# Optimization experiments

Measured on AMD Instinct MI355X. Metric: run time of the kernel, lower is better.

Reference implementation:

```python
import jax, jax.numpy as jnp
import numpy as np

NUM_HEADS = 8
NUM_GROUPS = 32
EPS = 1e-5


def group_norm(x, gamma, beta):
    b, c, h, w = x.shape
    xg = x.reshape(b, NUM_GROUPS, c // NUM_GROUPS, h, w)
    mean = jnp.mean(xg, axis=(2, 3, 4), keepdims=True)
    var = jnp.var(xg, axis=(2, 3, 4), keepdims=True)
    xn = ((xg - mean) * jax.lax.rsqrt(var + EPS)).reshape(b, c, h, w)
    return xn * gamma[None, :, None, None] + beta[None, :, None, None]


def setup_inputs() -> dict:
    key = jax.random.key(0)
    ks = jax.random.split(key, 4)
    b, c, h, w = 16, 512, 32, 32
    x = jax.random.normal(ks[0], (b, c, h, w), dtype=jnp.float32)
    gn_gamma = jnp.ones((c,), dtype=jnp.float32)
    gn_beta = jnp.zeros((c,), dtype=jnp.float32)
    qkv_w = jax.random.normal(ks[1], (3 * c, c), dtype=jnp.float32) * (1.0 / np.sqrt(c))
    qkv_b = jnp.zeros((3 * c,), dtype=jnp.float32)
    proj_w = jax.random.normal(ks[2], (c, c), dtype=jnp.float32) * (1.0 / np.sqrt(c))
    proj_b = jnp.zeros((c,), dtype=jnp.float32)
    return {"x": x, "gn_gamma": gn_gamma, "gn_beta": gn_beta,
            "qkv_w": qkv_w, "qkv_b": qkv_b, "proj_w": proj_w, "proj_b": proj_b}


def reference(x, gn_gamma, gn_beta, qkv_w, qkv_b, proj_w, proj_b):
    b, c, h, w = x.shape
    hd = c // NUM_HEADS
    hw = h * w

    xn = group_norm(x, gn_gamma, gn_beta)
    # 1x1 conv == channel matmul
    qkv = jnp.einsum('oc,bchw->bohw', qkv_w, xn) + qkv_b[None, :, None, None]
    q, k, v = jnp.split(qkv, 3, axis=1)
    q = q.reshape(b, NUM_HEADS, hd, hw)
    k = k.reshape(b, NUM_HEADS, hd, hw)
    v = v.reshape(b, NUM_HEADS, hd, hw)

    scale = 1.0 / np.sqrt(hd)
    attn = jnp.einsum('bhdt,bhds->bhts', q, k) * scale  # [b,H,hw,hw]
    attn = jax.nn.softmax(attn, axis=-1)
    h_attn = jnp.einsum('bhts,bhds->bhdt', attn, v).reshape(b, c, h, w)

    h_attn = jnp.einsum('oc,bchw->bohw', proj_w, h_attn) + proj_b[None, :, None, None]
    return x + h_attn
```

## Files before the change

kernel.cpp:

```cpp
#include <hip/hip_runtime.h>
#include <math.h>

#define NUM_HEADS 8
#define NUM_GROUPS 32
#define EPS 1e-5f

constexpr int B  = 16;
constexpr int C  = 512;
constexpr int HW = 1024;
constexpr int HD = 64;

typedef short bf16x8 __attribute__((ext_vector_type(8)));
typedef float f32x4  __attribute__((ext_vector_type(4)));

#define QSCALE 0.1803368801111f

__device__ inline unsigned short f2bf(float f) {
    union { float f; unsigned int u; } v; v.f = f;
    unsigned int r = (v.u + 0x7FFFu + ((v.u >> 16) & 1u)) >> 16;
    return (unsigned short)r;
}

__device__ __forceinline__ unsigned int pack_trunc(float lo, float hi) {
    return __builtin_amdgcn_perm(__float_as_uint(hi), __float_as_uint(lo), 0x07060302u);
}

__device__ __forceinline__ float exp2_raw(float x) {
#if __has_builtin(__builtin_amdgcn_exp2f)
    return __builtin_amdgcn_exp2f(x);
#else
    float r; asm("v_exp_f32 %0, %1" : "=v"(r) : "v"(x)); return r;
#endif
}

__device__ __forceinline__ void gld_lds16(void* lds, const void* g) {
    __builtin_amdgcn_global_load_lds(
        (const __attribute__((address_space(1))) void*)g,
        (__attribute__((address_space(3))) void*)lds, 16, 0, 0);
}

__device__ __forceinline__ void pl32_swap(unsigned int& a, unsigned int& b) {
#if __has_builtin(__builtin_amdgcn_permlane32_swap)
    auto r = __builtin_amdgcn_permlane32_swap(a, b, false, false);
    a = r[0]; b = r[1];
#else
    asm volatile("v_permlane32_swap_b32 %0, %1" : "+v"(a), "+v"(b));
#endif
}
__device__ __forceinline__ void pl16_swap(unsigned int& a, unsigned int& b) {
#if __has_builtin(__builtin_amdgcn_permlane16_swap)
    auto r = __builtin_amdgcn_permlane16_swap(a, b, false, false);
    a = r[0]; b = r[1];
#else
    asm volatile("v_permlane16_swap_b32 %0, %1" : "+v"(a), "+v"(b));
#endif
}

#define ABAR(VM) do {                                                   \
    asm volatile("s_waitcnt vmcnt(" VM ")\n\ts_barrier" ::: "memory");  \
    __builtin_amdgcn_sched_barrier(0);                                  \
} while (0)

__global__ __launch_bounds__(256)
void groupnorm_t_kernel(const float* __restrict__ x,
                        const float* __restrict__ gamma,
                        const float* __restrict__ beta,
                        unsigned short* __restrict__ xnT) {
    const int bg = blockIdx.x;
    const int b = bg >> 5, g = bg & 31;
    const size_t base = ((size_t)b * C + (size_t)g * 16) * HW;

    float v[4][16];
    float sum = 0.f, sumsq = 0.f;
    #pragma unroll
    for (int p = 0; p < 4; ++p) {
        const int t = threadIdx.x + p * 256;
        #pragma unroll
        for (int cl = 0; cl < 16; ++cl) {
            const float f = x[base + (size_t)cl * HW + t];
            v[p][cl] = f;
            sum += f;
            sumsq += f * f;
        }
    }
    #pragma unroll
    for (int off = 32; off > 0; off >>= 1) {
        sum   += __shfl_down(sum, off, 64);
        sumsq += __shfl_down(sumsq, off, 64);
    }
    __shared__ float s_sum[4], s_sq[4];
    const int wid = threadIdx.x >> 6, lane = threadIdx.x & 63;
    if (lane == 0) { s_sum[wid] = sum; s_sq[wid] = sumsq; }
    __syncthreads();
    const float tsum = s_sum[0] + s_sum[1] + s_sum[2] + s_sum[3];
    const float tsq  = s_sq[0] + s_sq[1] + s_sq[2] + s_sq[3];
    const float mean = tsum * (1.0f / 16384.f);
    const float var  = tsq * (1.0f / 16384.f) - mean * mean;
    const float rstd = rsqrtf(var + EPS);

    float ga[16], be[16];
    #pragma unroll
    for (int cl = 0; cl < 16; ++cl) {
        ga[cl] = gamma[g * 16 + cl] * rstd;
        be[cl] = beta[g * 16 + cl] - mean * ga[cl];
    }

    #pragma unroll
    for (int p = 0; p < 4; ++p) {
        const int t = threadIdx.x + p * 256;
        unsigned short pk[16];
        #pragma unroll
        for (int cl = 0; cl < 16; ++cl)
            pk[cl] = f2bf(v[p][cl] * ga[cl] + be[cl]);
        unsigned short* dst = xnT + ((size_t)(b * 1024 + t)) * 512 + g * 16;
        *(uint4*)dst = *(const uint4*)pk;
        *(uint4*)(dst + 8) = *(const uint4*)(pk + 8);
    }
}

__global__ __launch_bounds__(256)
void wconv_kernel(const float* __restrict__ qkv_w,
                  const float* __restrict__ proj_w,
                  unsigned short* __restrict__ wqb) {
    const int i = blockIdx.x * 256 + threadIdx.x;
    const int n1 = 786432 / 4;
    const int nt = 1048576 / 4;
    if (i >= nt) return;
    const float4 v = (i < n1) ? ((const float4*)qkv_w)[i]
                              : ((const float4*)proj_w)[i - n1];
    ushort4 r;
    r.x = f2bf(v.x); r.y = f2bf(v.y); r.z = f2bf(v.z); r.w = f2bf(v.w);
    ((ushort4*)wqb)[i] = r;
}

__device__ __forceinline__ void gemm_stage(const char* __restrict__ Ab,
                                           const char* __restrict__ Bb,
                                           int step, unsigned short* As,
                                           unsigned short* Bs,
                                           int w, int lrow, int lkc) {
    #pragma unroll
    for (int i = 0; i < 2; ++i) {
        const int row = w * 32 + i * 16 + lrow;
        const int kc = lkc ^ ((row >> 1) & 3);
        const size_t goff = (size_t)row * 1024 + (size_t)step * 64 + kc * 16;
        gld_lds16((char*)As + w * 2048 + i * 1024, Ab + goff);
        gld_lds16((char*)Bs + w * 2048 + i * 1024, Bb + goff);
    }
}

__device__ __forceinline__ void gemm_step(const unsigned short* __restrict__ As,
                                          const unsigned short* __restrict__ Bs,
                                          f32x4 acc[4][4],
                                          int lo, int q4, int wm, int wn) {
    bf16x8 af[4], bfr[4];
    #pragma unroll
    for (int i = 0; i < 4; ++i) {
        const int ra = wm * 64 + i * 16 + lo;
        af[i]  = *(const bf16x8*)(As + ra * 32 + (q4 ^ ((ra >> 1) & 3)) * 8);
        const int rb = wn * 64 + i * 16 + lo;
        bfr[i] = *(const bf16x8*)(Bs + rb * 32 + (q4 ^ ((rb >> 1) & 3)) * 8);
    }
    __builtin_amdgcn_s_setprio(1);
    #pragma unroll
    for (int mi = 0; mi < 4; ++mi)
        #pragma unroll
        for (int ni = 0; ni < 4; ++ni)
            acc[mi][ni] = __builtin_amdgcn_mfma_f32_16x16x32_bf16(
                af[mi], bfr[ni], acc[mi][ni], 0, 0, 0);
    __builtin_amdgcn_s_setprio(0);
}

__device__ __forceinline__ void mfma_gemm_pipe(const char* __restrict__ Ab,
                                               const char* __restrict__ Bb,
                                               unsigned short* S,
                                               f32x4 acc[4][4]) {
    const int tid = threadIdx.x;
    const int w = tid >> 6, lane = tid & 63;
    const int lo = lane & 15, q4 = lane >> 4;
    const int wm = w >> 1, wn = w & 1;
    const int lrow = lane >> 2, lkc = lane & 3;

    unsigned short* A0 = S;             unsigned short* B0 = S + 4096;
    unsigned short* A1 = S + 8192;      unsigned short* B1 = S + 12288;
    unsigned short* A2 = S + 16384;     unsigned short* B2 = S + 20480;

    gemm_stage(Ab, Bb, 0, A0, B0, w, lrow, lkc);
    gemm_stage(Ab, Bb, 1, A1, B1, w, lrow, lkc);
    ABAR("4");
    gemm_stage(Ab, Bb, 2, A2, B2, w, lrow, lkc);
    gemm_step(A0, B0, acc, lo, q4, wm, wn);

    #pragma unroll 1
    for (int ii = 0; ii < 4; ++ii) {
        const int i = 3 * ii + 1;
        ABAR("4");
        gemm_stage(Ab, Bb, i + 2, A0, B0, w, lrow, lkc);
        gemm_step(A1, B1, acc, lo, q4, wm, wn);
        ABAR("4");
        gemm_stage(Ab, Bb, i + 3, A1, B1, w, lrow, lkc);
        gemm_step(A2, B2, acc, lo, q4, wm, wn);
        ABAR("4");
        gemm_stage(Ab, Bb, i + 4, A2, B2, w, lrow, lkc);
        gemm_step(A0, B0, acc, lo, q4, wm, wn);
    }

    ABAR("4");
    gemm_stage(Ab, Bb, 15, A0, B0, w, lrow, lkc);
    gemm_step(A1, B1, acc, lo, q4, wm, wn);
    ABAR("4");
    gemm_step(A2, B2, acc, lo, q4, wm, wn);
    ABAR("0");
    gemm_step(A0, B0, acc, lo, q4, wm, wn);
}

__global__ __launch_bounds__(256)
void qkv_mfma_kernel(const unsigned short* __restrict__ wqb,
                     const unsigned short* __restrict__ xnT,
                     const float* __restrict__ qkv_b,
                     unsigned short* __restrict__ Qt,
                     unsigned short* __restrict__ Kt,
                     unsigned short* __restrict__ Vb) {
    __shared__ __align__(16) unsigned short SMEM[3 * 8192];
    const int batch = blockIdx.z;
    const int mBase = blockIdx.y * 128, nBase = blockIdx.x * 128;

    f32x4 acc[4][4] = {};
    mfma_gemm_pipe((const char*)(wqb + (size_t)mBase * 512),
                   (const char*)(xnT + ((size_t)batch * 1024 + nBase) * 512),
                   SMEM, acc);

    const int tid = threadIdx.x;
    const int w = tid >> 6, lane = tid & 63;
    const int lo = lane & 15, q4 = lane >> 4;
    const int wm = w >> 1, wn = w & 1;
    const int mw = mBase + wm * 64;
    const int tb = nBase + wn * 64;

    __syncthreads();

    if (mw < 1024) {
        const bool isQ = mw < 512;
        const int head = (mw >> 6) & 7;
        unsigned short* dst = (isQ ? Qt : Kt) + (((size_t)batch * 8 + head) << 16);
        const float sc = isQ ? QSCALE : 1.0f;
        #pragma unroll
        for (int mi = 0; mi < 4; ++mi) {
            const float4 bq = *(const float4*)(qkv_b + mw + mi * 16 + q4 * 4);
            #pragma unroll
            for (int ni = 0; ni < 4; ++ni) {
                const int t = tb + ni * 16 + lo;
                ushort4 pk;
                pk.x = f2bf((acc[mi][ni][0] + bq.x) * sc);
                pk.y = f2bf((acc[mi][ni][1] + bq.y) * sc);
                pk.z = f2bf((acc[mi][ni][2] + bq.z) * sc);
                pk.w = f2bf((acc[mi][ni][3] + bq.w) * sc);
                *(ushort4*)(dst + (size_t)t * 64 + mi * 16 + q4 * 4) = pk;
            }
        }
    } else {
        unsigned short* T = SMEM + w * 2048;
        unsigned short* Vrow = Vb + (size_t)batch * 524288 + (size_t)(mw - 1024) * 1024 + tb;
        const int rl8 = lane >> 3, c8 = lane & 7;
        #pragma unroll
        for (int p = 0; p < 2; ++p) {
            #pragma unroll
            for (int mi2 = 0; mi2 < 2; ++mi2) {
                const int mi = 2 * p + mi2;
                const float4 bq = *(const float4*)(qkv_b + mw + mi * 16 + q4 * 4);
                const int dl = mi2 * 16 + q4 * 4;
                #pragma unroll
                for (int ni = 0; ni < 4; ++ni) {
                    const int tl = ni * 16 + lo;
                    T[(dl + 0) * 64 + tl] = f2bf(acc[mi][ni][0] + bq.x);
                    T[(dl + 1) * 64 + tl] = f2bf(acc[mi][ni][1] + bq.y);
                    T[(dl + 2) * 64 + tl] = f2bf(acc[mi][ni][2] + bq.z);
                    T[(dl + 3) * 64 + tl] = f2bf(acc[mi][ni][3] + bq.w);
                }
            }
            #pragma unroll
            for (int i = 0; i < 4; ++i) {
                const int dl = i * 8 + rl8;
                const uint4 val = *(const uint4*)&T[dl * 64 + c8 * 8];
                *(uint4*)(Vrow + (size_t)(p * 32 + dl) * 1024 + c8 * 8) = val;
            }
        }
    }
}

__device__ __forceinline__ void attn_stage(const unsigned short* __restrict__ Kp,
                                           const unsigned short* __restrict__ Vp,
                                           int s0, unsigned short* Kd,
                                           unsigned short* Vd,
                                           int w, int rl, int p8) {
    #pragma unroll
    for (int cc = 0; cc < 2; ++cc) {
        const int r = 16 * w + 8 * cc + rl;
        const int jj = p8 ^ (r & 7);
        gld_lds16(Kd + (16 * w + 8 * cc) * 64, Kp + (size_t)(s0 + r) * 64 + jj * 8);
        gld_lds16(Vd + (16 * w + 8 * cc) * 64, Vp + (size_t)r * 1024 + s0 + jj * 8);
    }
}

__device__ __forceinline__ void attn_chunk(const unsigned short* __restrict__ Kc,
                                           const unsigned short* __restrict__ Vc,
                                           const bf16x8 (&qf)[2][2],
                                           f32x4 (&oacc)[4][2], float (&lrun)[2],
                                           int lo, int q4, int xr) {
    f32x4 sacc[4][2] = {};
    __builtin_amdgcn_s_setprio(1);
    #pragma unroll
    for (int mt = 0; mt < 4; ++mt) {
        const unsigned short* kr = Kc + (16 * mt + lo) * 64;
        const bf16x8 a0 = *(const bf16x8*)(kr + ((q4    ) ^ xr) * 8);
        const bf16x8 a1 = *(const bf16x8*)(kr + ((q4 + 4) ^ xr) * 8);
        #pragma unroll
        for (int nt = 0; nt < 2; ++nt) {
            sacc[mt][nt] = __builtin_amdgcn_mfma_f32_16x16x32_bf16(a0, qf[nt][0], sacc[mt][nt], 0, 0, 0);
            sacc[mt][nt] = __builtin_amdgcn_mfma_f32_16x16x32_bf16(a1, qf[nt][1], sacc[mt][nt], 0, 0, 0);
        }
    }
    __builtin_amdgcn_s_setprio(0);

    bf16x8 bp[2][2];
    #pragma unroll
    for (int nt = 0; nt < 2; ++nt) {
        unsigned int X[4][2];
        float ps = 0.f;
        #pragma unroll
        for (int mt = 0; mt < 4; ++mt) {
            const f32x4 s = sacc[mt][nt];
            const float p0 = exp2_raw(s[0]);
            const float p1 = exp2_raw(s[1]);
            const float p2 = exp2_raw(s[2]);
            const float p3 = exp2_raw(s[3]);
            ps += (p0 + p1) + (p2 + p3);
            X[mt][0] = pack_trunc(p0, p1);
            X[mt][1] = pack_trunc(p2, p3);
        }
        lrun[nt] += ps;
        #pragma unroll
        for (int h2 = 0; h2 < 2; ++h2) {
            unsigned int Y0, Y1, Y2, Y3;
            {
                unsigned int a = X[2 * h2][0], bb = X[2 * h2 + 1][0];
                pl32_swap(a, bb);
                pl16_swap(a, bb);
                Y0 = a; Y2 = bb;
            }
            {
                unsigned int a = X[2 * h2][1], bb = X[2 * h2 + 1][1];
                pl32_swap(a, bb);
                pl16_swap(a, bb);
                Y1 = a; Y3 = bb;
            }
            union { unsigned int u[4]; bf16x8 v; } cv;
            cv.u[0] = Y0; cv.u[1] = Y1; cv.u[2] = Y2; cv.u[3] = Y3;
            bp[nt][h2] = cv.v;
        }
    }

    __builtin_amdgcn_s_setprio(1);
    #pragma unroll
    for (int md = 0; md < 4; ++md) {
        const unsigned short* vr = Vc + (16 * md + lo) * 64;
        const bf16x8 v0 = *(const bf16x8*)(vr + ((q4    ) ^ xr) * 8);
        const bf16x8 v1 = *(const bf16x8*)(vr + ((q4 + 4) ^ xr) * 8);
        #pragma unroll
        for (int nt = 0; nt < 2; ++nt) {
            oacc[md][nt] = __builtin_amdgcn_mfma_f32_16x16x32_bf16(v0, bp[nt][0], oacc[md][nt], 0, 0, 0);
            oacc[md][nt] = __builtin_amdgcn_mfma_f32_16x16x32_bf16(v1, bp[nt][1], oacc[md][nt], 0, 0, 0);
        }
    }
    __builtin_amdgcn_s_setprio(0);
}

__global__ __launch_bounds__(256, 3)
void attn_mfma_kernel(const unsigned short* __restrict__ Qt,
                      const unsigned short* __restrict__ Kt,
                      const unsigned short* __restrict__ Vb,
                      unsigned short* __restrict__ attnT) {
    const int bh = blockIdx.x;
    const int b = bh >> 3, h = bh & 7;
    const int tBase = blockIdx.y * 128;
    const int tid = threadIdx.x;
    const int w = tid >> 6, lane = tid & 63;
    const int lo = lane & 15, q4 = lane >> 4;
    const int xr = lo & 7;

    __shared__ __align__(16) unsigned short Ks[3][64 * 64];
    __shared__ __align__(16) unsigned short Vs[3][64 * 64];

    const unsigned short* Kp = Kt + ((size_t)bh << 16);
    const unsigned short* Vp = Vb + ((size_t)b * 512 + h * 64) * 1024;

    bf16x8 qf[2][2];
    {
        const unsigned short* Qp = Qt + ((size_t)bh * 1024 + tBase + 32 * w) * 64;
        #pragma unroll
        for (int nt = 0; nt < 2; ++nt) {
            qf[nt][0] = *(const bf16x8*)(Qp + (size_t)(16 * nt + lo) * 64 + 8 * q4);
            qf[nt][1] = *(const bf16x8*)(Qp + (size_t)(16 * nt + lo) * 64 + 32 + 8 * q4);
        }
    }

    const int rl = lane >> 3, p8 = lane & 7;

    f32x4 oacc[4][2] = {};
    float lrun[2] = {0.f, 0.f};

    attn_stage(Kp, Vp, 0 * 64, Ks[0], Vs[0], w, rl, p8);
    attn_stage(Kp, Vp, 1 * 64, Ks[1], Vs[1], w, rl, p8);

    ABAR("4");
    attn_stage(Kp, Vp, 2 * 64, Ks[2], Vs[2], w, rl, p8);
    attn_chunk(Ks[0], Vs[0], qf, oacc, lrun, lo, q4, xr);

    #pragma unroll 1
    for (int ii = 0; ii < 4; ++ii) {
        const int i = 3 * ii + 1;
        ABAR("4");
        attn_stage(Kp, Vp, (i + 2) * 64, Ks[0], Vs[0], w, rl, p8);
        attn_chunk(Ks[1], Vs[1], qf, oacc, lrun, lo, q4, xr);
        ABAR("4");
        attn_stage(Kp, Vp, (i + 3) * 64, Ks[1], Vs[1], w, rl, p8);
        attn_chunk(Ks[2], Vs[2], qf, oacc, lrun, lo, q4, xr);
        ABAR("4");
        attn_stage(Kp, Vp, (i + 4) * 64, Ks[2], Vs[2], w, rl, p8);
        attn_chunk(Ks[0], Vs[0], qf, oacc, lrun, lo, q4, xr);
    }

    ABAR("4");
    attn_stage(Kp, Vp, 15 * 64, Ks[0], Vs[0], w, rl, p8);
    attn_chunk(Ks[1], Vs[1], qf, oacc, lrun, lo, q4, xr);
    ABAR("4");
    attn_chunk(Ks[2], Vs[2], qf, oacc, lrun, lo, q4, xr);
    ABAR("0");
    attn_chunk(Ks[0], Vs[0], qf, oacc, lrun, lo, q4, xr);

    #pragma unroll
    for (int nt = 0; nt < 2; ++nt) {
        float lt = lrun[nt];
        lt += __shfl_xor(lt, 16, 64);
        lt += __shfl_xor(lt, 32, 64);
        const float inv = 1.0f / lt;
        const int t = tBase + 32 * w + 16 * nt + lo;
        unsigned short* op = attnT + ((size_t)(b * 1024 + t)) * 512 + h * 64;
        #pragma unroll
        for (int md = 0; md < 4; ++md) {
            uint2 pk;
            pk.x = pack_trunc(oacc[md][nt][0] * inv, oacc[md][nt][1] * inv);
            pk.y = pack_trunc(oacc[md][nt][2] * inv, oacc[md][nt][3] * inv);
            *(uint2*)(op + 16 * md + 4 * q4) = pk;
        }
    }
}

__global__ __launch_bounds__(256)
void proj_mfma_kernel(const unsigned short* __restrict__ wpb,
                      const unsigned short* __restrict__ attnT,
                      const float* __restrict__ proj_b,
                      const float* __restrict__ x,
                      float* __restrict__ out) {
    __shared__ __align__(16) unsigned short SMEM[3 * 8192];
    const int batch = blockIdx.z;
    const int mBase = blockIdx.y * 128, nBase = blockIdx.x * 128;

    f32x4 acc[4][4] = {};
    mfma_gemm_pipe((const char*)(wpb + (size_t)mBase * 512),
                   (const char*)(attnT + ((size_t)batch * 1024 + nBase) * 512),
                   SMEM, acc);

    const int tid = threadIdx.x;
    const int w = tid >> 6, lane = tid & 63;
    const int lo = lane & 15, q4 = lane >> 4;
    const int wm = w >> 1, wn = w & 1;
    const float* xb = x + (size_t)batch * 524288;
    float* ob = out + (size_t)batch * 524288;

    #pragma unroll
    for (int mi = 0; mi < 4; ++mi) {
        const int m0 = mBase + wm * 64 + mi * 16 + q4 * 4;
        const float4 bq = *(const float4*)(proj_b + m0);
        #pragma unroll
        for (int ni = 0; ni < 4; ++ni) {
            const int t = nBase + wn * 64 + ni * 16 + lo;
            const size_t o0 = (size_t)m0 * 1024 + t;
            ob[o0]          = acc[mi][ni][0] + bq.x + xb[o0];
            ob[o0 + 1024]   = acc[mi][ni][1] + bq.y + xb[o0 + 1024];
            ob[o0 + 2048]   = acc[mi][ni][2] + bq.z + xb[o0 + 2048];
            ob[o0 + 3072]   = acc[mi][ni][3] + bq.w + xb[o0 + 3072];
        }
    }
}

extern "C" void kernel_launch(void* const* d_in, const int* in_sizes, int n_in,
                              void* d_out, int out_size, void* d_ws, size_t ws_size,
                              hipStream_t stream) {
    const float* x        = (const float*)d_in[0];
    const float* gn_gamma = (const float*)d_in[1];
    const float* gn_beta  = (const float*)d_in[2];
    const float* qkv_w    = (const float*)d_in[3];
    const float* qkv_b    = (const float*)d_in[4];
    const float* proj_w   = (const float*)d_in[5];
    const float* proj_b   = (const float*)d_in[6];
    float* out = (float*)d_out;

    char* wsc = (char*)d_ws;
    unsigned short* xnT   = (unsigned short*)(wsc);
    unsigned short* Qt    = (unsigned short*)(wsc + 16777216);
    unsigned short* Kt    = (unsigned short*)(wsc + 33554432);
    unsigned short* Vb    = (unsigned short*)(wsc + 50331648);
    unsigned short* attnT = (unsigned short*)(wsc + 67108864);
    unsigned short* wqb   = (unsigned short*)(wsc + 83886080);
    unsigned short* wpb   = wqb + 786432;

    groupnorm_t_kernel<<<B * NUM_GROUPS, 256, 0, stream>>>(x, gn_gamma, gn_beta, xnT);

    wconv_kernel<<<1024, 256, 0, stream>>>(qkv_w, proj_w, wqb);

    {
        dim3 grid(HW / 128, (3 * C) / 128, B);
        qkv_mfma_kernel<<<grid, 256, 0, stream>>>(wqb, xnT, qkv_b, Qt, Kt, Vb);
    }

    {
        dim3 grid(B * NUM_HEADS, HW / 128);
        attn_mfma_kernel<<<grid, 256, 0, stream>>>(Qt, Kt, Vb, attnT);
    }

    {
        dim3 grid(HW / 128, C / 128, B);
        proj_mfma_kernel<<<grid, 256, 0, stream>>>(wpb, attnT, proj_b, x, out);
    }
}
```

Before: 206.1 us.

## Fuse groupnorm with weight conversion and shrink attention V staging buffers

The groupnorm and weight bf16-conversion kernels are merged into one launch, with extra blocks doing the weight conversion, to save a launch and let the two run concurrently. The attention kernel now stages K two chunks ahead but V only one chunk ahead, using a 3-deep K ring and a 2-deep V ring. This cuts LDS use so launch bounds can rise from 3 to 4 blocks per CU, trading a shallower V prefetch and a more intricate buffer rotation for higher occupancy.

```diff
diff --git a/kernel.cpp b/kernel.cpp
--- a/kernel.cpp
+++ b/kernel.cpp
@@ -62,10 +62,25 @@
 } while (0)
 
 __global__ __launch_bounds__(256)
-void groupnorm_t_kernel(const float* __restrict__ x,
-                        const float* __restrict__ gamma,
-                        const float* __restrict__ beta,
-                        unsigned short* __restrict__ xnT) {
+void fused_pre_kernel(const float* __restrict__ x,
+                      const float* __restrict__ gamma,
+                      const float* __restrict__ beta,
+                      unsigned short* __restrict__ xnT,
+                      const float* __restrict__ qkv_w,
+                      const float* __restrict__ proj_w,
+                      unsigned short* __restrict__ wqb) {
+    if (blockIdx.x >= 512) {
+        const int i = (blockIdx.x - 512) * 256 + threadIdx.x;
+        const int n1 = 786432 / 4;
+        const int nt = 1048576 / 4;
+        if (i >= nt) return;
+        const float4 v = (i < n1) ? ((const float4*)qkv_w)[i]
+                                  : ((const float4*)proj_w)[i - n1];
+        ushort4 r;
+        r.x = f2bf(v.x); r.y = f2bf(v.y); r.z = f2bf(v.z); r.w = f2bf(v.w);
+        ((ushort4*)wqb)[i] = r;
+        return;
+    }
     const int bg = blockIdx.x;
     const int b = bg >> 5, g = bg & 31;
     const size_t base = ((size_t)b * C + (size_t)g * 16) * HW;
@@ -116,21 +131,6 @@
         *(uint4*)dst = *(const uint4*)pk;
         *(uint4*)(dst + 8) = *(const uint4*)(pk + 8);
     }
-}
-
-__global__ __launch_bounds__(256)
-void wconv_kernel(const float* __restrict__ qkv_w,
-                  const float* __restrict__ proj_w,
-                  unsigned short* __restrict__ wqb) {
-    const int i = blockIdx.x * 256 + threadIdx.x;
-    const int n1 = 786432 / 4;
-    const int nt = 1048576 / 4;
-    if (i >= nt) return;
-    const float4 v = (i < n1) ? ((const float4*)qkv_w)[i]
-                              : ((const float4*)proj_w)[i - n1];
-    ushort4 r;
-    r.x = f2bf(v.x); r.y = f2bf(v.y); r.z = f2bf(v.z); r.w = f2bf(v.w);
-    ((ushort4*)wqb)[i] = r;
 }
 
 __device__ __forceinline__ void gemm_stage(const char* __restrict__ Ab,
@@ -287,16 +287,23 @@
     }
 }
 
-__device__ __forceinline__ void attn_stage(const unsigned short* __restrict__ Kp,
-                                           const unsigned short* __restrict__ Vp,
-                                           int s0, unsigned short* Kd,
-                                           unsigned short* Vd,
-                                           int w, int rl, int p8) {
+__device__ __forceinline__ void stage_K(const unsigned short* __restrict__ Kp,
+                                        int s0, unsigned short* Kd,
+                                        int w, int rl, int p8) {
     #pragma unroll
     for (int cc = 0; cc < 2; ++cc) {
         const int r = 16 * w + 8 * cc + rl;
         const int jj = p8 ^ (r & 7);
         gld_lds16(Kd + (16 * w + 8 * cc) * 64, Kp + (size_t)(s0 + r) * 64 + jj * 8);
+    }
+}
+__device__ __forceinline__ void stage_V(const unsigned short* __restrict__ Vp,
+                                        int s0, unsigned short* Vd,
+                                        int w, int rl, int p8) {
+    #pragma unroll
+    for (int cc = 0; cc < 2; ++cc) {
+        const int r = 16 * w + 8 * cc + rl;
+        const int jj = p8 ^ (r & 7);
         gld_lds16(Vd + (16 * w + 8 * cc) * 64, Vp + (size_t)r * 1024 + s0 + jj * 8);
     }
 }
@@ -374,7 +381,7 @@
     __builtin_amdgcn_s_setprio(0);
 }
 
-__global__ __launch_bounds__(256, 3)
+__global__ __launch_bounds__(256, 4)
 void attn_mfma_kernel(const unsigned short* __restrict__ Qt,
                       const unsigned short* __restrict__ Kt,
                       const unsigned short* __restrict__ Vb,
@@ -388,7 +395,7 @@
     const int xr = lo & 7;
 
     __shared__ __align__(16) unsigned short Ks[3][64 * 64];
-    __shared__ __align__(16) unsigned short Vs[3][64 * 64];
+    __shared__ __align__(16) unsigned short Vs[2][64 * 64];
 
     const unsigned short* Kp = Kt + ((size_t)bh << 16);
     const unsigned short* Vp = Vb + ((size_t)b * 512 + h * 64) * 1024;
@@ -408,34 +415,53 @@
     f32x4 oacc[4][2] = {};
     float lrun[2] = {0.f, 0.f};
 
-    attn_stage(Kp, Vp, 0 * 64, Ks[0], Vs[0], w, rl, p8);
-    attn_stage(Kp, Vp, 1 * 64, Ks[1], Vs[1], w, rl, p8);
-
-    ABAR("4");
-    attn_stage(Kp, Vp, 2 * 64, Ks[2], Vs[2], w, rl, p8);
+    stage_V(Vp, 0 * 64, Vs[0], w, rl, p8);
+    stage_K(Kp, 0 * 64, Ks[0], w, rl, p8);
+    stage_K(Kp, 1 * 64, Ks[1], w, rl, p8);
+
+    ABAR("2");
+    stage_V(Vp, 1 * 64, Vs[1], w, rl, p8);
+    stage_K(Kp, 2 * 64, Ks[2], w, rl, p8);
     attn_chunk(Ks[0], Vs[0], qf, oacc, lrun, lo, q4, xr);
 
     #pragma unroll 1
-    for (int ii = 0; ii < 4; ++ii) {
-        const int i = 3 * ii + 1;
-        ABAR("4");
-        attn_stage(Kp, Vp, (i + 2) * 64, Ks[0], Vs[0], w, rl, p8);
+    for (int ii = 0; ii < 2; ++ii) {
+        const int i = 6 * ii + 1;
+        ABAR("2");
+        stage_V(Vp, (i + 1) * 64, Vs[0], w, rl, p8);
+        stage_K(Kp, (i + 2) * 64, Ks[0], w, rl, p8);
         attn_chunk(Ks[1], Vs[1], qf, oacc, lrun, lo, q4, xr);
-        ABAR("4");
-        attn_stage(Kp, Vp, (i + 3) * 64, Ks[1], Vs[1], w, rl, p8);
-        attn_chunk(Ks[2], Vs[2], qf, oacc, lrun, lo, q4, xr);
-        ABAR("4");
-        attn_stage(Kp, Vp, (i + 4) * 64, Ks[2], Vs[2], w, rl, p8);
+        ABAR("2");
+        stage_V(Vp, (i + 2) * 64, Vs[1], w, rl, p8);
+        stage_K(Kp, (i + 3) * 64, Ks[1], w, rl, p8);
+        attn_chunk(Ks[2], Vs[0], qf, oacc, lrun, lo, q4, xr);
+        ABAR("2");
+        stage_V(Vp, (i + 3) * 64, Vs[0], w, rl, p8);
+        stage_K(Kp, (i + 4) * 64, Ks[2], w, rl, p8);
+        attn_chunk(Ks[0], Vs[1], qf, oacc, lrun, lo, q4, xr);
+        ABAR("2");
+        stage_V(Vp, (i + 4) * 64, Vs[1], w, rl, p8);
+        stage_K(Kp, (i + 5) * 64, Ks[0], w, rl, p8);
+        attn_chunk(Ks[1], Vs[0], qf, oacc, lrun, lo, q4, xr);
+        ABAR("2");
+        stage_V(Vp, (i + 5) * 64, Vs[0], w, rl, p8);
+        stage_K(Kp, (i + 6) * 64, Ks[1], w, rl, p8);
+        attn_chunk(Ks[2], Vs[1], qf, oacc, lrun, lo, q4, xr);
+        ABAR("2");
+        stage_V(Vp, (i + 6) * 64, Vs[1], w, rl, p8);
+        stage_K(Kp, (i + 7) * 64, Ks[2], w, rl, p8);
         attn_chunk(Ks[0], Vs[0], qf, oacc, lrun, lo, q4, xr);
     }
 
-    ABAR("4");
-    attn_stage(Kp, Vp, 15 * 64, Ks[0], Vs[0], w, rl, p8);
+    ABAR("2");
+    stage_V(Vp, 14 * 64, Vs[0], w, rl, p8);
+    stage_K(Kp, 15 * 64, Ks[0], w, rl, p8);
     attn_chunk(Ks[1], Vs[1], qf, oacc, lrun, lo, q4, xr);
-    ABAR("4");
-    attn_chunk(Ks[2], Vs[2], qf, oacc, lrun, lo, q4, xr);
+    ABAR("2");
+    stage_V(Vp, 15 * 64, Vs[1], w, rl, p8);
+    attn_chunk(Ks[2], Vs[0], qf, oacc, lrun, lo, q4, xr);
     ABAR("0");
-    attn_chunk(Ks[0], Vs[0], qf, oacc, lrun, lo, q4, xr);
+    attn_chunk(Ks[0], Vs[1], qf, oacc, lrun, lo, q4, xr);
 
     #pragma unroll
     for (int nt = 0; nt < 2; ++nt) {
@@ -514,9 +540,8 @@
     unsigned short* wqb   = (unsigned short*)(wsc + 83886080);
     unsigned short* wpb   = wqb + 786432;
 
-    groupnorm_t_kernel<<<B * NUM_GROUPS, 256, 0, stream>>>(x, gn_gamma, gn_beta, xnT);
-
-    wconv_kernel<<<1024, 256, 0, stream>>>(qkv_w, proj_w, wqb);
+    fused_pre_kernel<<<1536, 256, 0, stream>>>(x, gn_gamma, gn_beta, xnT,
+                                               qkv_w, proj_w, wqb);
 
     {
         dim3 grid(HW / 128, (3 * C) / 128, B);
```

After: 232.0 us. +12.6%, slower.

## Fuse groupnorm with weight conversion and remap GEMM block indices for XCD locality

Applied to the files above, without the earlier changes.

Merges the groupnorm/transpose kernel and the weight bf16 conversion kernel into a single launch, using a blockIdx split so both run concurrently, which removes one launch and its tail. The QKV and projection GEMMs move to 1D grids with a remapped block index, (id % N) * 8 + id / N. This is meant to place blocks that share batch and weight tiles on the same XCD (chiplet) to improve L2 reuse. The cost is more index arithmetic, and the mapping relies on round-robin dispatch of blocks across the 8 XCDs.

```diff
diff --git a/kernel.cpp b/kernel.cpp
--- a/kernel.cpp
+++ b/kernel.cpp
@@ -62,10 +62,25 @@
 } while (0)
 
 __global__ __launch_bounds__(256)
-void groupnorm_t_kernel(const float* __restrict__ x,
-                        const float* __restrict__ gamma,
-                        const float* __restrict__ beta,
-                        unsigned short* __restrict__ xnT) {
+void fused_pre_kernel(const float* __restrict__ x,
+                      const float* __restrict__ gamma,
+                      const float* __restrict__ beta,
+                      unsigned short* __restrict__ xnT,
+                      const float* __restrict__ qkv_w,
+                      const float* __restrict__ proj_w,
+                      unsigned short* __restrict__ wqb) {
+    if (blockIdx.x >= 512) {
+        const int i = (blockIdx.x - 512) * 256 + threadIdx.x;
+        const int n1 = 786432 / 4;
+        const int nt = 1048576 / 4;
+        if (i >= nt) return;
+        const float4 v = (i < n1) ? ((const float4*)qkv_w)[i]
+                                  : ((const float4*)proj_w)[i - n1];
+        ushort4 r;
+        r.x = f2bf(v.x); r.y = f2bf(v.y); r.z = f2bf(v.z); r.w = f2bf(v.w);
+        ((ushort4*)wqb)[i] = r;
+        return;
+    }
     const int bg = blockIdx.x;
     const int b = bg >> 5, g = bg & 31;
     const size_t base = ((size_t)b * C + (size_t)g * 16) * HW;
@@ -116,21 +131,6 @@
         *(uint4*)dst = *(const uint4*)pk;
         *(uint4*)(dst + 8) = *(const uint4*)(pk + 8);
     }
-}
-
-__global__ __launch_bounds__(256)
-void wconv_kernel(const float* __restrict__ qkv_w,
-                  const float* __restrict__ proj_w,
-                  unsigned short* __restrict__ wqb) {
-    const int i = blockIdx.x * 256 + threadIdx.x;
-    const int n1 = 786432 / 4;
-    const int nt = 1048576 / 4;
-    if (i >= nt) return;
-    const float4 v = (i < n1) ? ((const float4*)qkv_w)[i]
-                              : ((const float4*)proj_w)[i - n1];
-    ushort4 r;
-    r.x = f2bf(v.x); r.y = f2bf(v.y); r.z = f2bf(v.z); r.w = f2bf(v.w);
-    ((ushort4*)wqb)[i] = r;
 }
 
 __device__ __forceinline__ void gemm_stage(const char* __restrict__ Ab,
@@ -221,8 +221,12 @@
                      unsigned short* __restrict__ Kt,
                      unsigned short* __restrict__ Vb) {
     __shared__ __align__(16) unsigned short SMEM[3 * 8192];
-    const int batch = blockIdx.z;
-    const int mBase = blockIdx.y * 128, nBase = blockIdx.x * 128;
+    const int hw_id = blockIdx.x;
+    const int wk = (hw_id % 192) * 8 + hw_id / 192;
+    const int bx = wk & 7;
+    const int by = (wk >> 3) % 12;
+    const int batch = wk / 96;
+    const int mBase = by * 128, nBase = bx * 128;
 
     f32x4 acc[4][4] = {};
     mfma_gemm_pipe((const char*)(wqb + (size_t)mBase * 512),
@@ -462,8 +466,12 @@
                       const float* __restrict__ x,
                       float* __restrict__ out) {
     __shared__ __align__(16) unsigned short SMEM[3 * 8192];
-    const int batch = blockIdx.z;
-    const int mBase = blockIdx.y * 128, nBase = blockIdx.x * 128;
+    const int hw_id = blockIdx.x;
+    const int wk = (hw_id % 64) * 8 + hw_id / 64;
+    const int bx = wk & 7;
+    const int by = (wk >> 3) & 3;
+    const int batch = wk >> 5;
+    const int mBase = by * 128, nBase = bx * 128;
 
     f32x4 acc[4][4] = {};
     mfma_gemm_pipe((const char*)(wpb + (size_t)mBase * 512),
@@ -514,22 +522,15 @@
     unsigned short* wqb   = (unsigned short*)(wsc + 83886080);
     unsigned short* wpb   = wqb + 786432;
 
-    groupnorm_t_kernel<<<B * NUM_GROUPS, 256, 0, stream>>>(x, gn_gamma, gn_beta, xnT);
-
-    wconv_kernel<<<1024, 256, 0, stream>>>(qkv_w, proj_w, wqb);
-
-    {
-        dim3 grid(HW / 128, (3 * C) / 128, B);
-        qkv_mfma_kernel<<<grid, 256, 0, stream>>>(wqb, xnT, qkv_b, Qt, Kt, Vb);
-    }
+    fused_pre_kernel<<<1536, 256, 0, stream>>>(x, gn_gamma, gn_beta, xnT,
+                                               qkv_w, proj_w, wqb);
+
+    qkv_mfma_kernel<<<1536, 256, 0, stream>>>(wqb, xnT, qkv_b, Qt, Kt, Vb);
 
     {
         dim3 grid(B * NUM_HEADS, HW / 128);
         attn_mfma_kernel<<<grid, 256, 0, stream>>>(Qt, Kt, Vb, attnT);
     }
 
-    {
-        dim3 grid(HW / 128, C / 128, B);
-        proj_mfma_kernel<<<grid, 256, 0, stream>>>(wpb, attnT, proj_b, x, out);
-    }
-}
+    proj_mfma_kernel<<<512, 256, 0, stream>>>(wpb, attnT, proj_b, x, out);
+}
```

Result: no change. 204.8 us (median of 2 runs) (-0.6%).
